# Performance work log

Hardware: AMD Instinct MI355X
Metric: run time of the kernel (lower is better)

## Reference

```python
import jax, jax.numpy as jnp
import numpy as np

DIM = 512
CHUNK = 64
LN_EPS = 1e-5


def setup_inputs() -> dict:
    key = jax.random.key(0)
    ks = jax.random.split(key, 9)
    B, S, D = 4, 4096, DIM
    x = jax.random.normal(ks[0], (B, S, D), dtype=jnp.float32)
    # Linear weights stored as [in, out] (equivalent to torch W.T)
    W_omega = jax.random.normal(ks[1], (D, D), dtype=jnp.float32) / np.sqrt(D)
    b_omega = jnp.zeros((D,), dtype=jnp.float32)
    log_scale = jnp.full((D,), np.log(0.1), dtype=jnp.float32)
    ln_gamma = jnp.ones((4 * D,), dtype=jnp.float32)
    ln_beta = jnp.zeros((4 * D,), dtype=jnp.float32)
    W1 = jax.random.normal(ks[2], (4 * D, 2 * D), dtype=jnp.float32) / np.sqrt(4 * D)
    b1 = jnp.zeros((2 * D,), dtype=jnp.float32)
    W2 = jax.random.normal(ks[3], (2 * D, D), dtype=jnp.float32) / np.sqrt(2 * D)
    b2 = jnp.zeros((D,), dtype=jnp.float32)
    return {"x": x, "W_omega": W_omega, "b_omega": b_omega, "log_scale": log_scale,
            "ln_gamma": ln_gamma, "ln_beta": ln_beta, "W1": W1, "b1": b1, "W2": W2, "b2": b2}


def reference(x, W_omega, b_omega, log_scale, ln_gamma, ln_beta, W1, b1, W2, b2):
    B, S, D = x.shape
    C = CHUNK
    # S chosen as multiple of C, so pad_len == 0 (matches torch no-pad branch)
    N = S // C
    omega = x @ W_omega + b_omega                      # [B,S,D]
    oc = omega.reshape(B, N, C, D)
    xc = x.reshape(B, N, C, D)
    pos = jnp.arange(1, C + 1, dtype=x.dtype)          # [C]
    pos_scale = (1.0 / jnp.sqrt(pos))[None, None, :, None]
    scale = jnp.exp(log_scale)
    phi = jnp.cumsum(oc * scale * pos_scale, axis=2)   # [B,N,C,D]
    cos_phi = jnp.cos(phi)
    sin_phi = jnp.sin(phi)
    cr = xc * cos_phi                                   # content modulated real
    ci = xc * sin_phi                                   # content modulated imag
    pos_norm = pos[None, None, :, None]
    mr = jnp.cumsum(cr, axis=2) / pos_norm              # memory real
    mi = jnp.cumsum(ci, axis=2) / pos_norm              # memory imag
    rr = mr * cos_phi + mi * sin_phi                    # retrieved real
    ri = mi * cos_phi - mr * sin_phi                    # retrieved imag
    ctx = jnp.concatenate([cr.reshape(B, S, D), ci.reshape(B, S, D),
                           rr.reshape(B, S, D), ri.reshape(B, S, D)], axis=-1)  # [B,S,4D]
    mu = jnp.mean(ctx, axis=-1, keepdims=True)
    var = jnp.mean((ctx - mu) ** 2, axis=-1, keepdims=True)
    h = (ctx - mu) / jnp.sqrt(var + LN_EPS) * ln_gamma + ln_beta
    h = h @ W1 + b1
    h = jax.nn.gelu(h, approximate=False)               # torch GELU default = exact erf
    out = h @ W2 + b2                                   # dropout is identity at eval
    return x + out
```

## Files before the change

kernel.cpp:

```cpp
#include <hip/hip_runtime.h>
#include <hip/hip_bf16.h>
#include <math.h>


typedef __bf16 bf16x8 __attribute__((ext_vector_type(8)));
typedef __bf16 bf16x4 __attribute__((ext_vector_type(4)));
typedef __bf16 bf16x2 __attribute__((ext_vector_type(2)));
typedef float  f32x4  __attribute__((ext_vector_type(4)));

typedef __attribute__((address_space(1))) void* gas_ptr;
typedef __attribute__((address_space(3))) void* las_ptr;

__device__ __forceinline__ void load_lds16(const void* g, void* l) {
    __builtin_amdgcn_global_load_lds((gas_ptr)g, (las_ptr)l, 16, 0, 0);
}

__device__ __forceinline__ void transpose_tile(const float* __restrict__ in,
                                               __bf16* __restrict__ out,
                                               int K, int N, int bx, int by,
                                               float (*tile)[33])
{
    const int tid = threadIdx.x;
    const int tx = tid & 31, ty = tid >> 5;
    const int n0 = bx * 32, k0 = by * 32;
    #pragma unroll
    for (int i = 0; i < 32; i += 8)
        tile[ty + i][tx] = in[(size_t)(k0 + ty + i) * N + n0 + tx];
    __syncthreads();
    #pragma unroll
    for (int i = 0; i < 32; i += 8)
        out[(size_t)(n0 + ty + i) * K + k0 + tx] = (__bf16)tile[tx][ty + i];
}

__global__ __launch_bounds__(256)
void prep_kernel(const float* __restrict__ x, __bf16* __restrict__ xb,
                 const float* __restrict__ W_omega, __bf16* __restrict__ womT,
                 const float* __restrict__ W1, __bf16* __restrict__ w1T,
                 const float* __restrict__ W2, __bf16* __restrict__ w2T)
{
    __shared__ float tile[32][33];
    const int bid = blockIdx.x;
    if (bid < 8192) {
        int i = bid * 256 + threadIdx.x;
        float4 v = ((const float4*)x)[i];
        bf16x4 o = { (__bf16)v.x, (__bf16)v.y, (__bf16)v.z, (__bf16)v.w };
        ((bf16x4*)xb)[i] = o;
    } else if (bid < 8448) {
        int t = bid - 8192;
        transpose_tile(W_omega, womT, 512, 512, t & 15, t >> 4, tile);
    } else if (bid < 10496) {
        int t = bid - 8448;
        transpose_tile(W1, w1T, 2048, 1024, t & 31, t >> 5, tile);
    } else {
        int t = bid - 10496;
        transpose_tile(W2, w2T, 1024, 512, t & 15, t >> 4, tile);
    }
}

template<int MODE>
__global__ __launch_bounds__(512, 1)
void gemm128_kernel(const __bf16* __restrict__ A, const __bf16* __restrict__ Bt,
                    const float* __restrict__ bias, const __bf16* __restrict__ resid,
                    void* __restrict__ out, int M, int N, int K)
{
    __shared__ __bf16 As[4][256 * 32];
    __shared__ __bf16 Bs[4][128 * 32];

    const int tid  = threadIdx.x;
    const int wv   = tid >> 6;
    const int lane = tid & 63;
    const int wm   = wv >> 1;
    const int wn   = wv & 1;

    const int tiles_n = N >> 7;
    const int ln_tn   = __ffs(tiles_n) - 1;
    const int per_m   = (M >> 8) >> 3;

    const int xcd = blockIdx.x & 7;
    const int j   = blockIdx.x >> 3;
    const int tile_m = (xcd * per_m + (j >> ln_tn)) << 8;
    const int tile_n = (j & (tiles_n - 1)) << 7;

    const int srow = 16 * wv + (lane >> 2);
    const int sig8 = (((lane & 3) ^ ((lane >> 3) & 3)) << 3);

    const __bf16* Ag = A  + (size_t)(tile_m + srow) * K + sig8;
    const __bf16* Bg = Bt + (size_t)(tile_n + srow) * K + sig8;
    const size_t rowK128 = (size_t)128 * K;
    const int lbase = wv * 512;

    const int lr    = lane & 15;
    const int q4    = lane >> 4;
    const int fslot = ((q4 ^ ((lane >> 1) & 3)) << 3);
    const int arow0 = wm * 64 + lr;
    const int brow0 = wn * 64 + lr;

    const unsigned ldsA0 = (unsigned)(size_t)(las_ptr)&As[0][0];
    const unsigned ldsB0 = (unsigned)(size_t)(las_ptr)&Bs[0][0];
    const unsigned asA = ldsA0 + (unsigned)((arow0 * 32 + fslot) << 1);
    const unsigned asB = ldsB0 + (unsigned)((brow0 * 32 + fslot) << 1);

    f32x4 acc[4][4];
    #pragma unroll
    for (int i = 0; i < 4; ++i)
        #pragma unroll
        for (int jj = 0; jj < 4; ++jj)
            acc[i][jj] = (f32x4){0.f, 0.f, 0.f, 0.f};

    const int NKS = K >> 5;

    auto stage = [&](int ks) {
        const int slot = ks & 3;
        const __bf16* ag = Ag + (ks << 5);
        const __bf16* bg = Bg + (ks << 5);
        load_lds16(ag,           &As[slot][lbase]);
        load_lds16(ag + rowK128, &As[slot][4096 + lbase]);
        load_lds16(bg,           &Bs[slot][lbase]);
    };

    bf16x8 afA[4], bqA[4], afB[4], bqB[4];

#define DSR(d, a, o) asm volatile("ds_read_b128 %0, %1 offset:" o \
                                  : "=v"(d) : "v"(a))
#define SB __builtin_amdgcn_sched_barrier(0)
#define MM4(CAF, CBQ, I)                                                      \
    acc[I][0] = __builtin_amdgcn_mfma_f32_16x16x32_bf16(CAF[I], CBQ[0], acc[I][0], 0, 0, 0); \
    acc[I][1] = __builtin_amdgcn_mfma_f32_16x16x32_bf16(CAF[I], CBQ[1], acc[I][1], 0, 0, 0); \
    acc[I][2] = __builtin_amdgcn_mfma_f32_16x16x32_bf16(CAF[I], CBQ[2], acc[I][2], 0, 0, 0); \
    acc[I][3] = __builtin_amdgcn_mfma_f32_16x16x32_bf16(CAF[I], CBQ[3], acc[I][3], 0, 0, 0);

#define G128_READ(KS, NAF, NBQ)                                               \
    {                                                                         \
        const unsigned aA_ = asA + (unsigned)(((KS) & 3) << 14);              \
        const unsigned aB_ = asB + (unsigned)(((KS) & 3) << 13);              \
        DSR(NAF[0], aA_, "0");    DSR(NAF[1], aA_, "1024");                   \
        DSR(NAF[2], aA_, "2048"); DSR(NAF[3], aA_, "3072");                   \
        DSR(NBQ[0], aB_, "0");    DSR(NBQ[1], aB_, "1024");                   \
        DSR(NBQ[2], aB_, "2048"); DSR(NBQ[3], aB_, "3072");                   \
    }

#define G128_PHASE_FULL(KS, CAF, CBQ, NAF, NBQ)                               \
    {                                                                         \
        const int ks_ = (KS);                                                 \
        asm volatile("s_waitcnt vmcnt(6)" ::: "memory");                      \
        __builtin_amdgcn_s_barrier();                                         \
        asm volatile("" ::: "memory");                                        \
        const int slot_ = (ks_ + 4) & 3;                                      \
        const __bf16* ag_ = Ag + ((ks_ + 4) << 5);                            \
        const __bf16* bg_ = Bg + ((ks_ + 4) << 5);                            \
        const unsigned aA_ = asA + (unsigned)(((ks_ + 1) & 3) << 14);         \
        const unsigned aB_ = asB + (unsigned)(((ks_ + 1) & 3) << 13);         \
        __builtin_amdgcn_s_setprio(1);                                        \
        load_lds16(ag_,           &As[slot_][lbase]);                         \
        MM4(CAF, CBQ, 0) SB;                                                  \
        load_lds16(ag_ + rowK128, &As[slot_][4096 + lbase]);                  \
        load_lds16(bg_,           &Bs[slot_][lbase]);                         \
        MM4(CAF, CBQ, 1) SB;                                                  \
        DSR(NAF[0], aA_, "0");    DSR(NAF[1], aA_, "1024");                   \
        DSR(NAF[2], aA_, "2048"); DSR(NAF[3], aA_, "3072");                   \
        MM4(CAF, CBQ, 2) SB;                                                  \
        DSR(NBQ[0], aB_, "0");    DSR(NBQ[1], aB_, "1024");                   \
        DSR(NBQ[2], aB_, "2048"); DSR(NBQ[3], aB_, "3072");                   \
        MM4(CAF, CBQ, 3)                                                      \
        __builtin_amdgcn_s_setprio(0);                                        \
        asm volatile("s_waitcnt lgkmcnt(0)" ::: "memory");                    \
        __builtin_amdgcn_sched_barrier(0);                                    \
    }

#define G128_PHASE_TAIL(KS, CAF, CBQ, NAF, NBQ)                               \
    {                                                                         \
        const int ks_ = (KS);                                                 \
        const int r_  = NKS - 1 - ks_;                                        \
        if (r_ >= 3)      asm volatile("s_waitcnt vmcnt(6)" ::: "memory");    \
        else if (r_ == 2) asm volatile("s_waitcnt vmcnt(3)" ::: "memory");    \
        else if (r_ == 1) asm volatile("s_waitcnt vmcnt(0)" ::: "memory");    \
        __builtin_amdgcn_s_barrier();                                         \
        asm volatile("" ::: "memory");                                        \
        if (ks_ + 4 < NKS) stage(ks_ + 4);                                    \
        if (ks_ + 1 < NKS) G128_READ(ks_ + 1, NAF, NBQ)                       \
        __builtin_amdgcn_s_setprio(1);                                        \
        _Pragma("unroll")                                                     \
        for (int i_ = 0; i_ < 4; ++i_)                                        \
            _Pragma("unroll")                                                 \
            for (int j_ = 0; j_ < 4; ++j_)                                    \
                acc[i_][j_] = __builtin_amdgcn_mfma_f32_16x16x32_bf16(        \
                    CAF[i_], CBQ[j_], acc[i_][j_], 0, 0, 0);                  \
        __builtin_amdgcn_s_setprio(0);                                        \
        asm volatile("s_waitcnt lgkmcnt(0)" ::: "memory");                    \
        __builtin_amdgcn_sched_barrier(0);                                    \
    }

    stage(0); stage(1); stage(2);
    asm volatile("s_waitcnt vmcnt(6)" ::: "memory");
    __builtin_amdgcn_s_barrier();
    asm volatile("" ::: "memory");
    stage(3);
    G128_READ(0, afA, bqA)
    asm volatile("s_waitcnt lgkmcnt(0)" ::: "memory");
    __builtin_amdgcn_sched_barrier(0);

    int ks = 0;
    for (; ks + 6 < NKS; ks += 2) {
        G128_PHASE_FULL(ks,     afA, bqA, afB, bqB)
        G128_PHASE_FULL(ks + 1, afB, bqB, afA, bqA)
    }
    for (; ks < NKS; ks += 2) {
        G128_PHASE_TAIL(ks,     afA, bqA, afB, bqB)
        G128_PHASE_TAIL(ks + 1, afB, bqB, afA, bqA)
    }

#undef G128_PHASE_FULL
#undef G128_PHASE_TAIL
#undef G128_READ
#undef MM4
#undef SB
#undef DSR

    const int orow0 = tile_m + wm * 64 + (q4 << 2);
    const int ocol0 = tile_n + wn * 64 + lr;
    #pragma unroll
    for (int i = 0; i < 4; ++i) {
        #pragma unroll
        for (int jj = 0; jj < 4; ++jj) {
            const int col = ocol0 + jj * 16;
            const float bv = bias[col];
            #pragma unroll
            for (int r = 0; r < 4; ++r) {
                const int row = orow0 + i * 16 + r;
                float v = acc[i][jj][r] + bv;
                size_t idx = (size_t)row * N + col;
                if (MODE == 0) {
                    ((__bf16*)out)[idx] = (__bf16)v;
                } else {
                    ((float*)out)[idx] = v + (float)resid[idx];
                }
            }
        }
    }
}

template<int MODE>
__global__ __launch_bounds__(512, 1)
void gemm256_kernel(const __bf16* __restrict__ A, const __bf16* __restrict__ Bt,
                    const float* __restrict__ bias, void* __restrict__ out,
                    int M, int N, int K)
{
    __shared__ __bf16 As[4][256 * 32];
    __shared__ __bf16 Bs[4][256 * 32];

    const int tid  = threadIdx.x;
    const int wv   = tid >> 6;
    const int lane = tid & 63;
    const int wm   = wv >> 2;
    const int wn   = wv & 3;

    const int tiles_n = N >> 8;
    const int ln_tn   = __ffs(tiles_n) - 1;
    const int per_m   = (M >> 8) >> 3;

    const int xcd = blockIdx.x & 7;
    const int j   = blockIdx.x >> 3;
    const int tile_m = (xcd * per_m + (j >> ln_tn)) << 8;
    const int tile_n = (j & (tiles_n - 1)) << 8;

    const int srow = 16 * wv + (lane >> 2);
    const int sig8 = (((lane & 3) ^ ((lane >> 3) & 3)) << 3);

    const __bf16* Ag = A  + (size_t)(tile_m + srow) * K + sig8;
    const __bf16* Bg = Bt + (size_t)(tile_n + srow) * K + sig8;
    const size_t rowK128 = (size_t)128 * K;
    const int lbase = wv * 512;

    const int lr    = lane & 15;
    const int q4    = lane >> 4;
    const int fslot = ((q4 ^ ((lane >> 1) & 3)) << 3);
    const int arow0 = wm * 128 + lr;
    const int brow0 = wn * 64 + lr;

    const unsigned ldsA0 = (unsigned)(size_t)(las_ptr)&As[0][0];
    const unsigned ldsB0 = (unsigned)(size_t)(las_ptr)&Bs[0][0];
    const unsigned asA = ldsA0 + (unsigned)((arow0 * 32 + fslot) << 1);
    const unsigned asB = ldsB0 + (unsigned)((brow0 * 32 + fslot) << 1);

    f32x4 acc[8][4];
    #pragma unroll
    for (int i = 0; i < 8; ++i)
        #pragma unroll
        for (int jj = 0; jj < 4; ++jj)
            acc[i][jj] = (f32x4){0.f, 0.f, 0.f, 0.f};

    const int NKS = K >> 5;

    auto stage = [&](int ks) {
        const int slot = ks & 3;
        const __bf16* ag = Ag + (ks << 5);
        const __bf16* bg = Bg + (ks << 5);
        load_lds16(ag,           &As[slot][lbase]);
        load_lds16(ag + rowK128, &As[slot][4096 + lbase]);
        load_lds16(bg,           &Bs[slot][lbase]);
        load_lds16(bg + rowK128, &Bs[slot][4096 + lbase]);
    };

    bf16x8 afA[8], bqA[4], afB[8], bqB[4];

#define DSR(d, a, o) asm volatile("ds_read_b128 %0, %1 offset:" o \
                                  : "=v"(d) : "v"(a))
#define SB __builtin_amdgcn_sched_barrier(0)
#define MM4(CAF, CBQ, I)                                                      \
    acc[I][0] = __builtin_amdgcn_mfma_f32_16x16x32_bf16(CAF[I], CBQ[0], acc[I][0], 0, 0, 0); \
    acc[I][1] = __builtin_amdgcn_mfma_f32_16x16x32_bf16(CAF[I], CBQ[1], acc[I][1], 0, 0, 0); \
    acc[I][2] = __builtin_amdgcn_mfma_f32_16x16x32_bf16(CAF[I], CBQ[2], acc[I][2], 0, 0, 0); \
    acc[I][3] = __builtin_amdgcn_mfma_f32_16x16x32_bf16(CAF[I], CBQ[3], acc[I][3], 0, 0, 0);

#define G256_READ(KS, NAF, NBQ)                                               \
    {                                                                         \
        const unsigned aA_ = asA + (unsigned)(((KS) & 3) << 14);              \
        const unsigned aB_ = asB + (unsigned)(((KS) & 3) << 14);              \
        DSR(NAF[0], aA_, "0");    DSR(NAF[1], aA_, "1024");                   \
        DSR(NAF[2], aA_, "2048"); DSR(NAF[3], aA_, "3072");                   \
        DSR(NAF[4], aA_, "4096"); DSR(NAF[5], aA_, "5120");                   \
        DSR(NAF[6], aA_, "6144"); DSR(NAF[7], aA_, "7168");                   \
        DSR(NBQ[0], aB_, "0");    DSR(NBQ[1], aB_, "1024");                   \
        DSR(NBQ[2], aB_, "2048"); DSR(NBQ[3], aB_, "3072");                   \
    }

#define G256_PHASE_FULL(KS, CAF, CBQ, NAF, NBQ)                               \
    {                                                                         \
        const int ks_ = (KS);                                                 \
        asm volatile("s_waitcnt vmcnt(8)" ::: "memory");                      \
        __builtin_amdgcn_s_barrier();                                         \
        asm volatile("" ::: "memory");                                        \
        const int slot_ = (ks_ + 4) & 3;                                      \
        const __bf16* ag_ = Ag + ((ks_ + 4) << 5);                            \
        const __bf16* bg_ = Bg + ((ks_ + 4) << 5);                            \
        const unsigned aA_ = asA + (unsigned)(((ks_ + 1) & 3) << 14);         \
        const unsigned aB_ = asB + (unsigned)(((ks_ + 1) & 3) << 14);         \
        __builtin_amdgcn_s_setprio(1);                                        \
        load_lds16(ag_,           &As[slot_][lbase]);                         \
        MM4(CAF, CBQ, 0) SB;                                                  \
        load_lds16(ag_ + rowK128, &As[slot_][4096 + lbase]);                  \
        MM4(CAF, CBQ, 1) SB;                                                  \
        load_lds16(bg_,           &Bs[slot_][lbase]);                         \
        MM4(CAF, CBQ, 2) SB;                                                  \
        load_lds16(bg_ + rowK128, &Bs[slot_][4096 + lbase]);                  \
        MM4(CAF, CBQ, 3) SB;                                                  \
        DSR(NAF[0], aA_, "0"); DSR(NAF[1], aA_, "1024");                      \
        DSR(NAF[2], aA_, "2048");                                             \
        MM4(CAF, CBQ, 4) SB;                                                  \
        DSR(NAF[3], aA_, "3072"); DSR(NAF[4], aA_, "4096");                   \
        DSR(NAF[5], aA_, "5120");                                             \
        MM4(CAF, CBQ, 5) SB;                                                  \
        DSR(NAF[6], aA_, "6144"); DSR(NAF[7], aA_, "7168");                   \
        DSR(NBQ[0], aB_, "0");                                                \
        MM4(CAF, CBQ, 6) SB;                                                  \
        DSR(NBQ[1], aB_, "1024"); DSR(NBQ[2], aB_, "2048");                   \
        DSR(NBQ[3], aB_, "3072");                                             \
        MM4(CAF, CBQ, 7)                                                      \
        __builtin_amdgcn_s_setprio(0);                                        \
        asm volatile("s_waitcnt lgkmcnt(0)" ::: "memory");                    \
        __builtin_amdgcn_sched_barrier(0);                                    \
    }

#define G256_PHASE_TAIL(KS, CAF, CBQ, NAF, NBQ)                               \
    {                                                                         \
        const int ks_ = (KS);                                                 \
        const int r_  = NKS - 1 - ks_;                                        \
        if (r_ >= 3)      asm volatile("s_waitcnt vmcnt(8)" ::: "memory");    \
        else if (r_ == 2) asm volatile("s_waitcnt vmcnt(4)" ::: "memory");    \
        else if (r_ == 1) asm volatile("s_waitcnt vmcnt(0)" ::: "memory");    \
        __builtin_amdgcn_s_barrier();                                         \
        asm volatile("" ::: "memory");                                        \
        if (ks_ + 4 < NKS) stage(ks_ + 4);                                    \
        if (ks_ + 1 < NKS) G256_READ(ks_ + 1, NAF, NBQ)                       \
        __builtin_amdgcn_s_setprio(1);                                        \
        _Pragma("unroll")                                                     \
        for (int i_ = 0; i_ < 8; ++i_)                                        \
            _Pragma("unroll")                                                 \
            for (int j_ = 0; j_ < 4; ++j_)                                    \
                acc[i_][j_] = __builtin_amdgcn_mfma_f32_16x16x32_bf16(        \
                    CAF[i_], CBQ[j_], acc[i_][j_], 0, 0, 0);                  \
        __builtin_amdgcn_s_setprio(0);                                        \
        asm volatile("s_waitcnt lgkmcnt(0)" ::: "memory");                    \
        __builtin_amdgcn_sched_barrier(0);                                    \
    }

    stage(0); stage(1); stage(2);
    asm volatile("s_waitcnt vmcnt(8)" ::: "memory");
    __builtin_amdgcn_s_barrier();
    asm volatile("" ::: "memory");
    stage(3);
    G256_READ(0, afA, bqA)
    asm volatile("s_waitcnt lgkmcnt(0)" ::: "memory");
    __builtin_amdgcn_sched_barrier(0);

    int ks = 0;
    for (; ks + 6 < NKS; ks += 2) {
        G256_PHASE_FULL(ks,     afA, bqA, afB, bqB)
        G256_PHASE_FULL(ks + 1, afB, bqB, afA, bqA)
    }
    for (; ks < NKS; ks += 2) {
        G256_PHASE_TAIL(ks,     afA, bqA, afB, bqB)
        G256_PHASE_TAIL(ks + 1, afB, bqB, afA, bqA)
    }

#undef G256_PHASE_FULL
#undef G256_PHASE_TAIL
#undef G256_READ
#undef MM4
#undef SB
#undef DSR

    const int orow0 = tile_m + wm * 128 + (q4 << 2);
    const int ocol0 = tile_n + wn * 64 + lr;
    #pragma unroll
    for (int i = 0; i < 8; ++i) {
        #pragma unroll
        for (int jj = 0; jj < 4; ++jj) {
            const int col = ocol0 + jj * 16;
            const float bv = bias[col];
            #pragma unroll
            for (int r = 0; r < 4; ++r) {
                const int row = orow0 + i * 16 + r;
                float v = acc[i][jj][r] + bv;
                if (MODE == 1) {
                    float g = 0.5f * v * (1.0f + erff(v * 0.70710678118654752f));
                    ((__bf16*)out)[(size_t)row * N + col] = (__bf16)g;
                } else {
                    ((__bf16*)out)[(size_t)row * N + col] = (__bf16)v;
                }
            }
        }
    }
}

__global__ __launch_bounds__(256)
void scan_ln_kernel(const __bf16* __restrict__ xb, const __bf16* __restrict__ omega,
                    const float* __restrict__ log_scale,
                    const float* __restrict__ gamma, const float* __restrict__ beta,
                    __bf16* __restrict__ ctx)
{
    const int chunk = blockIdx.x;
    const int tid   = threadIdx.x;
    const int lane  = tid & 63, wv = tid >> 6;
    const int d0    = tid << 1;
    const size_t base = (size_t)chunk * 64 * 512;

    float scale[2], g0[2], g1[2], g2[2], g3[2], e0[2], e1[2], e2[2], e3[2];
    #pragma unroll
    for (int u = 0; u < 2; ++u) {
        const int d = d0 + u;
        scale[u] = expf(log_scale[d]);
        g0[u] = gamma[d]; g1[u] = gamma[512 + d]; g2[u] = gamma[1024 + d]; g3[u] = gamma[1536 + d];
        e0[u] = beta[d];  e1[u] = beta[512 + d];  e2[u] = beta[1024 + d];  e3[u] = beta[1536 + d];
    }

    float phi[2] = {0.f, 0.f}, scr[2] = {0.f, 0.f}, sci[2] = {0.f, 0.f};
    __shared__ float red[2][8];

    bf16x2 om_n = *(const bf16x2*)&omega[base + d0];
    bf16x2 xv_n = *(const bf16x2*)&xb[base + d0];

    for (int c = 0; c < 64; ++c) {
        const bf16x2 omv = om_n;
        const bf16x2 xvv = xv_n;
        if (c < 63) {
            om_n = *(const bf16x2*)&omega[base + (size_t)(c + 1) * 512 + d0];
            xv_n = *(const bf16x2*)&xb[base + (size_t)(c + 1) * 512 + d0];
        }
        const float rsq = rsqrtf((float)(c + 1));
        const float inv = 1.0f / (float)(c + 1);

        float cr[2], ci[2], rr[2], ri[2];
        float s = 0.f, s2 = 0.f;
        #pragma unroll
        for (int u = 0; u < 2; ++u) {
            const float om = (float)omv[u];
            const float xv = (float)xvv[u];
            phi[u] += om * scale[u] * rsq;
            float sp, cp;
            __sincosf(phi[u], &sp, &cp);
            cr[u] = xv * cp; ci[u] = xv * sp;
            scr[u] += cr[u]; sci[u] += ci[u];
            const float mr = scr[u] * inv, mi = sci[u] * inv;
            rr[u] = mr * cp + mi * sp;
            ri[u] = mi * cp - mr * sp;
            s  += cr[u] + ci[u] + rr[u] + ri[u];
            s2 += cr[u]*cr[u] + ci[u]*ci[u] + rr[u]*rr[u] + ri[u]*ri[u];
        }
        #pragma unroll
        for (int o = 32; o > 0; o >>= 1) {
            s  += __shfl_xor(s, o);
            s2 += __shfl_xor(s2, o);
        }
        if (lane == 0) { red[c & 1][wv] = s; red[c & 1][4 + wv] = s2; }
        __syncthreads();
        const float S  = red[c & 1][0] + red[c & 1][1] + red[c & 1][2] + red[c & 1][3];
        const float S2 = red[c & 1][4] + red[c & 1][5] + red[c & 1][6] + red[c & 1][7];
        const float mu   = S * (1.0f / 2048.0f);
        const float var  = S2 * (1.0f / 2048.0f) - mu * mu;
        const float rstd = rsqrtf(var + 1e-5f);

        const size_t ob = ((size_t)chunk * 64 + c) * 2048;
        bf16x2 o0, o1, o2, o3;
        #pragma unroll
        for (int u = 0; u < 2; ++u) {
            o0[u] = (__bf16)(((cr[u] - mu) * rstd) * g0[u] + e0[u]);
            o1[u] = (__bf16)(((ci[u] - mu) * rstd) * g1[u] + e1[u]);
            o2[u] = (__bf16)(((rr[u] - mu) * rstd) * g2[u] + e2[u]);
            o3[u] = (__bf16)(((ri[u] - mu) * rstd) * g3[u] + e3[u]);
        }
        *(bf16x2*)&ctx[ob + d0]        = o0;
        *(bf16x2*)&ctx[ob + 512 + d0]  = o1;
        *(bf16x2*)&ctx[ob + 1024 + d0] = o2;
        *(bf16x2*)&ctx[ob + 1536 + d0] = o3;
    }
}

extern "C" void kernel_launch(void* const* d_in, const int* in_sizes, int n_in,
                              void* d_out, int out_size, void* d_ws, size_t ws_size,
                              hipStream_t stream)
{
    const float* x         = (const float*)d_in[0];
    const float* W_omega   = (const float*)d_in[1];
    const float* b_omega   = (const float*)d_in[2];
    const float* log_scale = (const float*)d_in[3];
    const float* ln_gamma  = (const float*)d_in[4];
    const float* ln_beta   = (const float*)d_in[5];
    const float* W1        = (const float*)d_in[6];
    const float* b1        = (const float*)d_in[7];
    const float* W2        = (const float*)d_in[8];
    const float* b2        = (const float*)d_in[9];
    float* out = (float*)d_out;

    char* ws = (char*)d_ws;
    __bf16* xb    = (__bf16*)(ws);
    __bf16* womT  = (__bf16*)(ws + 16777216);
    __bf16* w1T   = (__bf16*)(ws + 17301504);
    __bf16* w2T   = (__bf16*)(ws + 21495808);
    __bf16* omega = (__bf16*)(ws + 22544384);
    __bf16* hbuf  = (__bf16*)(ws + 22544384);
    __bf16* ctx   = (__bf16*)(ws + 56098816);

    prep_kernel<<<11008, 256, 0, stream>>>(x, xb, W_omega, womT, W1, w1T, W2, w2T);

    gemm128_kernel<0><<<256, 512, 0, stream>>>(xb, womT, b_omega, nullptr, omega, 16384, 512, 512);

    scan_ln_kernel<<<256, 256, 0, stream>>>(xb, omega, log_scale, ln_gamma, ln_beta, ctx);

    gemm256_kernel<1><<<256, 512, 0, stream>>>(ctx, w1T, b1, hbuf, 16384, 1024, 2048);

    gemm128_kernel<2><<<256, 512, 0, stream>>>(hbuf, w2T, b2, xb, out, 16384, 512, 1024);
}
```

Measured before the change: 258.8 us.

## Fold LayerNorm into W1 GEMM epilogue via gamma-scaled weights and row stats

LayerNorm normalization is moved out of the scan kernel. Gamma is folded into the transposed W1, and precomputed column sums u=gamma·W1 and v=beta·W1 plus per-row (rstd, mu*rstd) are applied in the W1 GEMM epilogue. The scan kernel now writes raw context values and uses one thread per dim with 512 threads, replacing the per-step block barrier with a single reduction at the end. The cost is bf16 rounding of unnormalized context and a subtraction in the epilogue, which can lose precision. The prep kernel also gains extra blocks with a serial 256-step dot product.

```diff
diff --git a/kernel.cpp b/kernel.cpp
--- a/kernel.cpp
+++ b/kernel.cpp
@@ -18,7 +18,8 @@
 __device__ __forceinline__ void transpose_tile(const float* __restrict__ in,
                                                __bf16* __restrict__ out,
                                                int K, int N, int bx, int by,
-                                               float (*tile)[33])
+                                               float (*tile)[33],
+                                               const float* __restrict__ colscale)
 {
     const int tid = threadIdx.x;
     const int tx = tid & 31, ty = tid >> 5;
@@ -27,18 +28,22 @@
     for (int i = 0; i < 32; i += 8)
         tile[ty + i][tx] = in[(size_t)(k0 + ty + i) * N + n0 + tx];
     __syncthreads();
+    const float cs = colscale ? colscale[k0 + tx] : 1.0f;
     #pragma unroll
     for (int i = 0; i < 32; i += 8)
-        out[(size_t)(n0 + ty + i) * K + k0 + tx] = (__bf16)tile[tx][ty + i];
+        out[(size_t)(n0 + ty + i) * K + k0 + tx] = (__bf16)(tile[tx][ty + i] * cs);
 }
 
 __global__ __launch_bounds__(256)
 void prep_kernel(const float* __restrict__ x, __bf16* __restrict__ xb,
                  const float* __restrict__ W_omega, __bf16* __restrict__ womT,
                  const float* __restrict__ W1, __bf16* __restrict__ w1T,
-                 const float* __restrict__ W2, __bf16* __restrict__ w2T)
+                 const float* __restrict__ W2, __bf16* __restrict__ w2T,
+                 const float* __restrict__ gamma, const float* __restrict__ beta,
+                 float* __restrict__ ubuf, float* __restrict__ vbuf)
 {
     __shared__ float tile[32][33];
+    __shared__ float uv[32][8][2];
     const int bid = blockIdx.x;
     if (bid < 8192) {
         int i = bid * 256 + threadIdx.x;
@@ -47,13 +52,35 @@
         ((bf16x4*)xb)[i] = o;
     } else if (bid < 8448) {
         int t = bid - 8192;
-        transpose_tile(W_omega, womT, 512, 512, t & 15, t >> 4, tile);
+        transpose_tile(W_omega, womT, 512, 512, t & 15, t >> 4, tile, nullptr);
     } else if (bid < 10496) {
         int t = bid - 8448;
-        transpose_tile(W1, w1T, 2048, 1024, t & 31, t >> 5, tile);
+        transpose_tile(W1, w1T, 2048, 1024, t & 31, t >> 5, tile, gamma);
+    } else if (bid < 11008) {
+        int t = bid - 10496;
+        transpose_tile(W2, w2T, 1024, 512, t & 15, t >> 4, tile, nullptr);
     } else {
-        int t = bid - 10496;
-        transpose_tile(W2, w2T, 1024, 512, t & 15, t >> 4, tile);
+        const int b  = bid - 11008;
+        const int nl = threadIdx.x & 31;
+        const int st = threadIdx.x >> 5;
+        const int n  = b * 32 + nl;
+        float su = 0.f, sv = 0.f;
+        const int k0 = st * 256;
+        for (int kk = 0; kk < 256; ++kk) {
+            const int k = k0 + kk;
+            const float w = W1[(size_t)k * 1024 + n];
+            su += gamma[k] * w;
+            sv += beta[k] * w;
+        }
+        uv[nl][st][0] = su; uv[nl][st][1] = sv;
+        __syncthreads();
+        if (threadIdx.x < 32) {
+            float U = 0.f, V = 0.f;
+            #pragma unroll
+            for (int s = 0; s < 8; ++s) { U += uv[threadIdx.x][s][0]; V += uv[threadIdx.x][s][1]; }
+            ubuf[b * 32 + threadIdx.x] = U;
+            vbuf[b * 32 + threadIdx.x] = V;
+        }
     }
 }
 
@@ -239,11 +266,11 @@
     }
 }
 
-template<int MODE>
 __global__ __launch_bounds__(512, 1)
 void gemm256_kernel(const __bf16* __restrict__ A, const __bf16* __restrict__ Bt,
-                    const float* __restrict__ bias, void* __restrict__ out,
-                    int M, int N, int K)
+                    const float* __restrict__ bias, const float* __restrict__ ubuf,
+                    const float* __restrict__ vbuf, const float2* __restrict__ musig,
+                    __bf16* __restrict__ out, int M, int N, int K)
 {
     __shared__ __bf16 As[4][256 * 32];
     __shared__ __bf16 Bs[4][256 * 32];
@@ -414,105 +441,85 @@
     const int ocol0 = tile_n + wn * 64 + lr;
     #pragma unroll
     for (int i = 0; i < 8; ++i) {
+        float2 ms[4];
+        #pragma unroll
+        for (int r = 0; r < 4; ++r)
+            ms[r] = musig[orow0 + i * 16 + r];
         #pragma unroll
         for (int jj = 0; jj < 4; ++jj) {
             const int col = ocol0 + jj * 16;
-            const float bv = bias[col];
+            const float u_c  = ubuf[col];
+            const float vb_c = vbuf[col] + bias[col];
             #pragma unroll
             for (int r = 0; r < 4; ++r) {
                 const int row = orow0 + i * 16 + r;
-                float v = acc[i][jj][r] + bv;
-                if (MODE == 1) {
-                    float g = 0.5f * v * (1.0f + erff(v * 0.70710678118654752f));
-                    ((__bf16*)out)[(size_t)row * N + col] = (__bf16)g;
-                } else {
-                    ((__bf16*)out)[(size_t)row * N + col] = (__bf16)v;
-                }
+                const float z = ms[r].x * acc[i][jj][r] - ms[r].y * u_c + vb_c;
+                const float g = 0.5f * z * (1.0f + erff(z * 0.70710678118654752f));
+                out[(size_t)row * N + col] = (__bf16)g;
             }
         }
     }
 }
 
-__global__ __launch_bounds__(256)
-void scan_ln_kernel(const __bf16* __restrict__ xb, const __bf16* __restrict__ omega,
-                    const float* __restrict__ log_scale,
-                    const float* __restrict__ gamma, const float* __restrict__ beta,
-                    __bf16* __restrict__ ctx)
+__global__ __launch_bounds__(512)
+void scan_raw_kernel(const __bf16* __restrict__ xb, const __bf16* __restrict__ omega,
+                     const float* __restrict__ log_scale,
+                     __bf16* __restrict__ ctx, float2* __restrict__ musig)
 {
     const int chunk = blockIdx.x;
-    const int tid   = threadIdx.x;
-    const int lane  = tid & 63, wv = tid >> 6;
-    const int d0    = tid << 1;
+    const int d     = threadIdx.x;
+    const int lane  = d & 63, wv = d >> 6;
     const size_t base = (size_t)chunk * 64 * 512;
 
-    float scale[2], g0[2], g1[2], g2[2], g3[2], e0[2], e1[2], e2[2], e3[2];
-    #pragma unroll
-    for (int u = 0; u < 2; ++u) {
-        const int d = d0 + u;
-        scale[u] = expf(log_scale[d]);
-        g0[u] = gamma[d]; g1[u] = gamma[512 + d]; g2[u] = gamma[1024 + d]; g3[u] = gamma[1536 + d];
-        e0[u] = beta[d];  e1[u] = beta[512 + d];  e2[u] = beta[1024 + d];  e3[u] = beta[1536 + d];
-    }
-
-    float phi[2] = {0.f, 0.f}, scr[2] = {0.f, 0.f}, sci[2] = {0.f, 0.f};
-    __shared__ float red[2][8];
-
-    bf16x2 om_n = *(const bf16x2*)&omega[base + d0];
-    bf16x2 xv_n = *(const bf16x2*)&xb[base + d0];
+    const float scale = expf(log_scale[d]);
+    float phi = 0.f, scr = 0.f, sci = 0.f;
+
+    __shared__ float2 psum[64][8];
+
+    float om_n = (float)omega[base + d];
+    float xv_n = (float)xb[base + d];
 
     for (int c = 0; c < 64; ++c) {
-        const bf16x2 omv = om_n;
-        const bf16x2 xvv = xv_n;
+        const float om = om_n;
+        const float xv = xv_n;
         if (c < 63) {
-            om_n = *(const bf16x2*)&omega[base + (size_t)(c + 1) * 512 + d0];
-            xv_n = *(const bf16x2*)&xb[base + (size_t)(c + 1) * 512 + d0];
+            om_n = (float)omega[base + (size_t)(c + 1) * 512 + d];
+            xv_n = (float)xb[base + (size_t)(c + 1) * 512 + d];
         }
-        const float rsq = rsqrtf((float)(c + 1));
+        phi += om * scale * rsqrtf((float)(c + 1));
+        float sp, cp;
+        __sincosf(phi, &sp, &cp);
+        const float cr = xv * cp, ci = xv * sp;
+        scr += cr; sci += ci;
         const float inv = 1.0f / (float)(c + 1);
-
-        float cr[2], ci[2], rr[2], ri[2];
-        float s = 0.f, s2 = 0.f;
-        #pragma unroll
-        for (int u = 0; u < 2; ++u) {
-            const float om = (float)omv[u];
-            const float xv = (float)xvv[u];
-            phi[u] += om * scale[u] * rsq;
-            float sp, cp;
-            __sincosf(phi[u], &sp, &cp);
-            cr[u] = xv * cp; ci[u] = xv * sp;
-            scr[u] += cr[u]; sci[u] += ci[u];
-            const float mr = scr[u] * inv, mi = sci[u] * inv;
-            rr[u] = mr * cp + mi * sp;
-            ri[u] = mi * cp - mr * sp;
-            s  += cr[u] + ci[u] + rr[u] + ri[u];
-            s2 += cr[u]*cr[u] + ci[u]*ci[u] + rr[u]*rr[u] + ri[u]*ri[u];
-        }
+        const float mr = scr * inv, mi = sci * inv;
+        const float rr = mr * cp + mi * sp;
+        const float ri = mi * cp - mr * sp;
+
+        const size_t ob = ((size_t)chunk * 64 + c) * 2048;
+        ctx[ob + d]        = (__bf16)cr;
+        ctx[ob + 512 + d]  = (__bf16)ci;
+        ctx[ob + 1024 + d] = (__bf16)rr;
+        ctx[ob + 1536 + d] = (__bf16)ri;
+
+        float s  = cr + ci + rr + ri;
+        float s2 = cr * cr + ci * ci + rr * rr + ri * ri;
         #pragma unroll
         for (int o = 32; o > 0; o >>= 1) {
             s  += __shfl_xor(s, o);
             s2 += __shfl_xor(s2, o);
         }
-        if (lane == 0) { red[c & 1][wv] = s; red[c & 1][4 + wv] = s2; }
-        __syncthreads();
-        const float S  = red[c & 1][0] + red[c & 1][1] + red[c & 1][2] + red[c & 1][3];
-        const float S2 = red[c & 1][4] + red[c & 1][5] + red[c & 1][6] + red[c & 1][7];
+        if (lane == 0) psum[c][wv] = make_float2(s, s2);
+    }
+    __syncthreads();
+    if (d < 64) {
+        float S = 0.f, S2 = 0.f;
+        #pragma unroll
+        for (int w = 0; w < 8; ++w) { S += psum[d][w].x; S2 += psum[d][w].y; }
         const float mu   = S * (1.0f / 2048.0f);
         const float var  = S2 * (1.0f / 2048.0f) - mu * mu;
         const float rstd = rsqrtf(var + 1e-5f);
-
-        const size_t ob = ((size_t)chunk * 64 + c) * 2048;
-        bf16x2 o0, o1, o2, o3;
-        #pragma unroll
-        for (int u = 0; u < 2; ++u) {
-            o0[u] = (__bf16)(((cr[u] - mu) * rstd) * g0[u] + e0[u]);
-            o1[u] = (__bf16)(((ci[u] - mu) * rstd) * g1[u] + e1[u]);
-            o2[u] = (__bf16)(((rr[u] - mu) * rstd) * g2[u] + e2[u]);
-            o3[u] = (__bf16)(((ri[u] - mu) * rstd) * g3[u] + e3[u]);
-        }
-        *(bf16x2*)&ctx[ob + d0]        = o0;
-        *(bf16x2*)&ctx[ob + 512 + d0]  = o1;
-        *(bf16x2*)&ctx[ob + 1024 + d0] = o2;
-        *(bf16x2*)&ctx[ob + 1536 + d0] = o3;
+        musig[chunk * 64 + d] = make_float2(rstd, mu * rstd);
     }
 }
 
@@ -540,14 +547,19 @@
     __bf16* omega = (__bf16*)(ws + 22544384);
     __bf16* hbuf  = (__bf16*)(ws + 22544384);
     __bf16* ctx   = (__bf16*)(ws + 56098816);
-
-    prep_kernel<<<11008, 256, 0, stream>>>(x, xb, W_omega, womT, W1, w1T, W2, w2T);
+    float2* musig = (float2*)(ws + 123207680);
+    float*  ubuf  = (float*)(ws + 123338752);
+    float*  vbuf  = (float*)(ws + 123342848);
+
+    prep_kernel<<<11040, 256, 0, stream>>>(x, xb, W_omega, womT, W1, w1T, W2, w2T,
+                                           ln_gamma, ln_beta, ubuf, vbuf);
 
     gemm128_kernel<0><<<256, 512, 0, stream>>>(xb, womT, b_omega, nullptr, omega, 16384, 512, 512);
 
-    scan_ln_kernel<<<256, 256, 0, stream>>>(xb, omega, log_scale, ln_gamma, ln_beta, ctx);
-
-    gemm256_kernel<1><<<256, 512, 0, stream>>>(ctx, w1T, b1, hbuf, 16384, 1024, 2048);
+    scan_raw_kernel<<<256, 512, 0, stream>>>(xb, omega, log_scale, ctx, musig);
+
+    gemm256_kernel<<<256, 512, 0, stream>>>(ctx, w1T, b1, ubuf, vbuf, musig,
+                                            hbuf, 16384, 1024, 2048);
 
     gemm128_kernel<2><<<256, 512, 0, stream>>>(hbuf, w2T, b2, xb, out, 16384, 512, 1024);
 }
```

Result: no change. 255.9 us (-1.1%).
